# Performance work log

Hardware: AMD Instinct MI355X
Metric: run time of the kernel (lower is better)

## Reference

```python
import jax, jax.numpy as jnp
import numpy as np

HEADS = 16
NUM_CHUNKS = 8  # min(int(log2(4096))+1, 8)


def setup_inputs() -> dict:
    key = jax.random.key(0)
    ks = jax.random.split(key, 6)
    B, T, C = 4, 4096, 1024
    s = 1.0 / np.sqrt(C)
    x = jax.random.normal(ks[0], (B, T, C), jnp.float32)
    Wqkv = jax.random.normal(ks[1], (3 * C, C), jnp.float32) * s
    Wout = jax.random.normal(ks[2], (C, C), jnp.float32) * s
    bout = jnp.zeros((C,), jnp.float32)
    Wl1 = jax.random.normal(ks[3], (64, 1), jnp.float32)
    bl1 = jnp.zeros((64,), jnp.float32)
    Wl2 = jax.random.normal(ks[4], (HEADS, 64), jnp.float32) * 0.125
    bl2 = jnp.zeros((HEADS,), jnp.float32)
    return dict(x=x, Wqkv=Wqkv, Wout=Wout, bout=bout, Wl1=Wl1, bl1=bl1, Wl2=Wl2, bl2=bl2)


def reference(x, Wqkv, Wout, bout, Wl1, bl1, Wl2, bl2):
    B, T, C = x.shape
    H = HEADS
    dh = C // H
    nc = NUM_CHUNKS
    cs = T // nc
    scale = dh ** (-0.5)

    # qkv projection (torch Linear: x @ W.T), split, to [B,H,T,dh]
    qkv = x @ Wqkv.T  # [B,T,3C]
    q, k, v = jnp.split(qkv, 3, axis=-1)
    def heads(t):
        return t.reshape(B, T, H, dh).transpose(0, 2, 1, 3)
    q, k, v = heads(q), heads(k), heads(v)

    # lambda gates from log positions: [T,1] -> [T,H] -> [H,T]
    log_pos = jnp.log(jnp.arange(T, dtype=jnp.float32) + 1.0)[:, None]
    h1 = jax.nn.relu(log_pos @ Wl1.T + bl1)            # [T,64]
    lam = jax.nn.sigmoid(h1 @ Wl2.T + bl2).T           # [H,T]
    lam = lam.reshape(H, nc, cs)                        # per-chunk key gates

    # block-local (chunked) attention, fully vectorized over chunks
    qc = q.reshape(B, H, nc, cs, dh)
    kc = k.reshape(B, H, nc, cs, dh)
    vc = v.reshape(B, H, nc, cs, dh)
    scores = jnp.einsum('bhnqd,bhnkd->bhnqk', qc, kc) * scale
    scores = scores * lam[None, :, :, None, :]          # gate keys pre-softmax
    attn = jax.nn.softmax(scores, axis=-1)
    out = jnp.einsum('bhnqk,bhnkd->bhnqd', attn, vc)    # [B,H,nc,cs,dh]

    out = out.reshape(B, H, T, dh).transpose(0, 2, 1, 3).reshape(B, T, C)
    return out @ Wout.T + bout
```

## Files before the change

### kernel.cpp

```cpp
#include <hip/hip_runtime.h>
#include <hip/hip_bf16.h>

typedef unsigned short u16;
typedef __attribute__((ext_vector_type(8))) short v8s;
typedef __attribute__((ext_vector_type(4))) float v4f;
typedef __attribute__((ext_vector_type(16))) float v16f;
typedef __attribute__((ext_vector_type(4))) unsigned v4u;

#define DEV __device__ __forceinline__

DEV u16 f2bf(float f) {
  union { float f; unsigned u; } v; v.f = f;
  unsigned r = v.u + 0x7fffu + ((v.u >> 16) & 1u);
  return (u16)(r >> 16);
}

DEV unsigned pk2bf(float a, float b) {
  float2 t; t.x = a; t.y = b;
  __hip_bfloat162 p = __float22bfloat162_rn(t);
  union { __hip_bfloat162 h; unsigned u; } c; c.h = p;
  return c.u;
}

DEV void gload_lds16(const void* g, void* l) {
  __builtin_amdgcn_global_load_lds(
      (const __attribute__((address_space(1))) void*)g,
      (__attribute__((address_space(3))) void*)l, 16, 0, 0);
}

__global__ __launch_bounds__(256) void cvt_bf16(const float* __restrict__ in,
                                                u16* __restrict__ out, int n4) {
  int i = blockIdx.x * 256 + threadIdx.x;
  if (i >= n4) return;
  float4 v = ((const float4*)in)[i];
  ushort4 o;
  o.x = f2bf(v.x); o.y = f2bf(v.y); o.z = f2bf(v.z); o.w = f2bf(v.w);
  ((ushort4*)out)[i] = o;
}

__global__ __launch_bounds__(256) void lam_kernel(const float* __restrict__ Wl1,
    const float* __restrict__ bl1, const float* __restrict__ Wl2,
    const float* __restrict__ bl2, float* __restrict__ lam) {
  int t = blockIdx.x * 256 + threadIdx.x;
  float lp = logf((float)t + 1.0f);
  float h1[64];
#pragma unroll
  for (int j = 0; j < 64; ++j) h1[j] = fmaxf(lp * Wl1[j] + bl1[j], 0.0f);
#pragma unroll 1
  for (int h = 0; h < 16; ++h) {
    float z = bl2[h];
#pragma unroll
    for (int j = 0; j < 64; ++j) z += h1[j] * Wl2[h * 64 + j];
    lam[h * 4096 + t] = 0.125f / (1.0f + expf(-z));
  }
}

template <int MH>
DEV void mfma32(v4f (&acc)[8][4], const v8s (&a)[4][2], const v8s (&b)[4][2]) {
#pragma unroll
  for (int kk = 0; kk < 2; ++kk)
#pragma unroll
    for (int i = 0; i < 4; ++i)
#pragma unroll
      for (int j = 0; j < 4; ++j)
        acc[MH * 4 + i][j] = __builtin_amdgcn_mfma_f32_16x16x32_bf16(
            a[i][kk], b[j][kk], acc[MH * 4 + i][j], 0, 0, 0);
}

DEV void ldA(v8s (&a)[4][2], const u16* Ab, int wr, int mh, int lane) {
  const int l15 = lane & 15, g = lane >> 4;
#pragma unroll
  for (int i = 0; i < 4; ++i) {
    const int row = wr * 128 + mh * 64 + i * 16 + l15;
#pragma unroll
    for (int kk = 0; kk < 2; ++kk)
      a[i][kk] = *(const v8s*)(Ab + row * 64 + (((kk * 4 + g) ^ (row & 7)) << 3));
  }
}

DEV void ldB4(v8s (&b)[4][2], const u16* Bb, int wc, int lane) {
  const int l15 = lane & 15, g = lane >> 4;
#pragma unroll
  for (int j = 0; j < 4; ++j) {
    const int row = (j >> 1) * 128 + wc * 32 + (j & 1) * 16 + l15;
#pragma unroll
    for (int kk = 0; kk < 2; ++kk)
      b[j][kk] = *(const v8s*)(Bb + row * 64 + (((kk * 4 + g) ^ (row & 7)) << 3));
  }
}

template <int OUTF32>
__global__ __launch_bounds__(512, 2) void gemm256(const u16* __restrict__ A,
    const u16* __restrict__ Bt, void* __restrict__ Cout,
    const float* __restrict__ bias, int M, int N, int K) {
  __shared__ u16 As[2][256 * 64];
  __shared__ u16 Bs[2][256 * 64];
  const int tid = threadIdx.x;
  const int lane = tid & 63;
  const int nbn = N >> 8;
  const int nwg = gridDim.x;
  int wg = blockIdx.x;
  wg = (wg & 7) * (nwg >> 3) + (wg >> 3);
  const int m0 = (wg / nbn) << 8;
  const int n0 = (wg % nbn) << 8;
  const int wid = tid >> 6;
  const int wr = wid >> 2;
  const int wc = wid & 3;
  const int nkt = K >> 6;
  const int nit = nkt >> 1;

  auto SAu = [&](int buf, int kt, int u) {
    const int ur = tid >> 3;
    const int slot = (tid & 7) ^ (ur & 7);
    gload_lds16(A + (size_t)(m0 + u * 64 + ur) * K + kt * 64 + slot * 8,
                &As[buf][u * 4096 + (tid & ~63) * 8]);
  };
  auto SBu = [&](int buf, int kt, int u) {
    const int q = tid >> 3;
    const int grow = (((u & 1) * 2 + (q >> 5)) << 6) + ((u >> 1) << 5) + (q & 31);
    const int slot = (tid & 7) ^ (q & 7);
    gload_lds16(Bt + (size_t)(n0 + grow) * K + kt * 64 + slot * 8,
                &Bs[buf][u * 4096 + (tid & ~63) * 8]);
  };
  auto SA_ = [&](int buf, int kt, int mh) { SAu(buf, kt, mh); SAu(buf, kt, 2 + mh); };
  auto SB_ = [&](int buf, int kt, int nh) { SBu(buf, kt, nh * 2); SBu(buf, kt, nh * 2 + 1); };

  v4f acc[8][4] = {};
  v8s a0[4][2], a1[4][2], b[4][2];

  SA_(0, 0, 0); SA_(0, 0, 1); SB_(0, 0, 0); SB_(0, 0, 1);
  SA_(1, 1, 0); SB_(1, 1, 0); SB_(1, 1, 1);
  asm volatile("s_waitcnt vmcnt(6)" ::: "memory");
  asm volatile("s_barrier" ::: "memory");

#define PHASE(MHc, AREG, VM, ...)                           \
  do { __VA_ARGS__; } while (0);                            \
  __builtin_amdgcn_s_setprio(1);                            \
  mfma32<MHc>(acc, AREG, b);                                \
  __builtin_amdgcn_s_setprio(0);                            \
  if (VM) asm volatile("s_waitcnt vmcnt(6)" ::: "memory");  \
  asm volatile("s_barrier" ::: "memory");

  for (int it = 0; it < nit; ++it) {
    const int t0 = 2 * it;
    const int t1 = t0 + 1;
    const int t2 = (t0 + 2 < nkt) ? t0 + 2 : nkt - 1;
    const int t3 = (t0 + 3 < nkt) ? t0 + 3 : nkt - 1;
    ldA(a0, As[0], wr, 0, lane); ldB4(b, Bs[0], wc, lane);
    ldA(a1, As[0], wr, 1, lane);
    PHASE(0, a0, 0, SAu(1, t1, 1); SAu(1, t1, 3));
    PHASE(1, a1, 1, SB_(0, t2, 0); SB_(0, t2, 1); SAu(0, t2, 0); SAu(0, t2, 2));
    ldA(a0, As[1], wr, 0, lane); ldB4(b, Bs[1], wc, lane);
    ldA(a1, As[1], wr, 1, lane);
    PHASE(0, a0, 0, SAu(0, t2, 1); SAu(0, t2, 3));
    PHASE(1, a1, 1, SB_(1, t3, 0); SB_(1, t3, 1); SAu(1, t3, 0); SAu(1, t3, 2));
  }
#undef PHASE

  const int l15 = lane & 15, g4 = (lane >> 4) * 4;
#pragma unroll
  for (int i = 0; i < 8; ++i) {
#pragma unroll
    for (int j = 0; j < 4; ++j) {
      const int gr = m0 + wr * 128 + i * 16 + g4;
      const int gc = n0 + wc * 64 + j * 16 + l15;
      float bv = OUTF32 ? bias[gc] : 0.0f;
#pragma unroll
      for (int r = 0; r < 4; ++r) {
        float val = acc[i][j][r];
        if (OUTF32) ((float*)Cout)[(size_t)(gr + r) * N + gc] = val + bv;
        else ((u16*)Cout)[(size_t)(gr + r) * N + gc] = f2bf(val);
      }
    }
  }
}

__global__ __launch_bounds__(1024, 4) void attn_chunk(const u16* __restrict__ qkv,
    const float* __restrict__ lam, u16* __restrict__ aout) {
  __shared__ u16 Ksm[512 * 64];
  __shared__ u16 Vt[64 * 520];
  __shared__ float lam_s[512];

  const int tid = threadIdx.x;
  const int lane = tid & 63;
  const int wid = tid >> 6;
  const int blk = blockIdx.x;
  const int c = blk & 7;
  const int hd = (blk >> 3) & 15;
  const int b = blk >> 7;
  const size_t tok0 = (size_t)b * 4096 + c * 512;
  const u16* qb = qkv + tok0 * 3072 + hd * 64;
  const u16* kb = qb + 1024;
  const u16* vb = qb + 2048;

  if (tid < 512) lam_s[tid] = lam[hd * 4096 + c * 512 + tid];

#pragma unroll
  for (int i = 0; i < 4; ++i) {
    const int r = i * 128 + wid * 8 + (lane >> 3);
    const int f = (r & 3) | (((r >> 3) & 1) << 2);
    gload_lds16(kb + (size_t)r * 3072 + (((lane & 7) ^ f) << 3),
                &Ksm[(i * 128 + wid * 8) * 64]);
  }
  {
    const int pr = tid & 255;
    const int k0 = 2 * pr;
    const int kg = k0 & 31;
    const int col = (k0 & ~31) + (kg & 16) + (((kg >> 2) & 1) << 3) +
                    ((kg & 3) | ((kg & 8) >> 1));
    const int db0 = (tid >> 8) * 2;
#pragma unroll
    for (int dbi = 0; dbi < 2; ++dbi) {
      const int d0 = (db0 + dbi) * 8;
      v8s v0 = *(const v8s*)(vb + (size_t)k0 * 3072 + d0);
      v8s v1 = *(const v8s*)(vb + (size_t)(k0 + 1) * 3072 + d0);
#pragma unroll
      for (int j = 0; j < 8; ++j) {
        unsigned pk = (unsigned)(u16)v0[j] | ((unsigned)(u16)v1[j] << 16);
        *(unsigned*)&Vt[(d0 + j) * 520 + col] = pk;
      }
    }
  }
  __syncthreads();

  const int l31 = lane & 31;
  const int hf = lane >> 5;
  const int fk = (l31 & 3) | (((l31 >> 3) & 1) << 2);

  const int q0 = wid * 32;
  v8s qv[4];
#pragma unroll
  for (int dsec = 0; dsec < 4; ++dsec)
    qv[dsec] = *(const v8s*)(qb + (size_t)(q0 + l31) * 3072 + dsec * 16 + hf * 8);

  float m = -1e30f, sum = 0.0f;
  v16f o0 = {}, o1 = {};

#pragma unroll 1
  for (int kt = 0; kt < 16; ++kt) {
    v16f acc = {};
#pragma unroll
    for (int dsec = 0; dsec < 4; ++dsec) {
      const v8s kf = *(const v8s*)&Ksm[(kt * 32 + l31) * 64 +
                                       (((dsec * 2 + hf) ^ fk) << 3)];
      acc = __builtin_amdgcn_mfma_f32_32x32x16_bf16(kf, qv[dsec], acc, 0, 0, 0);
    }
#pragma unroll
    for (int a = 0; a < 4; ++a) {
      const v4f lv = *(const v4f*)&lam_s[kt * 32 + a * 8 + hf * 4];
#pragma unroll
      for (int i = 0; i < 4; ++i) acc[4 * a + i] *= lv[i];
    }
    float tm = acc[0];
#pragma unroll
    for (int r = 1; r < 16; ++r) tm = fmaxf(tm, acc[r]);
    tm = fmaxf(tm, __shfl_xor(tm, 32));
    if (!__all(tm <= m + 8.0f)) {
      const float nm = fmaxf(m, tm);
      const float sc = __expf(m - nm);
      sum *= sc;
      o0 *= sc; o1 *= sc;
      m = nm;
    }
    float ps = 0.0f;
#pragma unroll
    for (int r = 0; r < 16; ++r) { acc[r] = __expf(acc[r] - m); ps += acc[r]; }
    sum += ps;
    v4u pa, pb;
    pa.x = pk2bf(acc[0], acc[1]);   pa.y = pk2bf(acc[2], acc[3]);
    pa.z = pk2bf(acc[4], acc[5]);   pa.w = pk2bf(acc[6], acc[7]);
    pb.x = pk2bf(acc[8], acc[9]);   pb.y = pk2bf(acc[10], acc[11]);
    pb.z = pk2bf(acc[12], acc[13]); pb.w = pk2bf(acc[14], acc[15]);
    const v8s pfA = __builtin_bit_cast(v8s, pa);
    const v8s pfB = __builtin_bit_cast(v8s, pb);
    const int vcol = kt * 32 + hf * 8;
    const v8s vA0 = *(const v8s*)&Vt[l31 * 520 + vcol];
    const v8s vB0 = *(const v8s*)&Vt[l31 * 520 + vcol + 16];
    const v8s vA1 = *(const v8s*)&Vt[(32 + l31) * 520 + vcol];
    const v8s vB1 = *(const v8s*)&Vt[(32 + l31) * 520 + vcol + 16];
    o0 = __builtin_amdgcn_mfma_f32_32x32x16_bf16(vA0, pfA, o0, 0, 0, 0);
    o0 = __builtin_amdgcn_mfma_f32_32x32x16_bf16(vB0, pfB, o0, 0, 0, 0);
    o1 = __builtin_amdgcn_mfma_f32_32x32x16_bf16(vA1, pfA, o1, 0, 0, 0);
    o1 = __builtin_amdgcn_mfma_f32_32x32x16_bf16(vB1, pfB, o1, 0, 0, 0);
  }

  sum += __shfl_xor(sum, 32);
  const float sv = 1.0f / sum;

  const size_t obase = (tok0 + q0 + l31) * 1024 + hd * 64;
#pragma unroll
  for (int a = 0; a < 4; ++a) {
    ushort4 w0, w1;
    w0.x = f2bf(o0[4 * a + 0] * sv); w0.y = f2bf(o0[4 * a + 1] * sv);
    w0.z = f2bf(o0[4 * a + 2] * sv); w0.w = f2bf(o0[4 * a + 3] * sv);
    w1.x = f2bf(o1[4 * a + 0] * sv); w1.y = f2bf(o1[4 * a + 1] * sv);
    w1.z = f2bf(o1[4 * a + 2] * sv); w1.w = f2bf(o1[4 * a + 3] * sv);
    *(ushort4*)&aout[obase + 8 * a + 4 * hf] = w0;
    *(ushort4*)&aout[obase + 32 + 8 * a + 4 * hf] = w1;
  }
}

extern "C" void kernel_launch(void* const* d_in, const int* in_sizes, int n_in,
                              void* d_out, int out_size, void* d_ws, size_t ws_size,
                              hipStream_t stream) {
  const float* x    = (const float*)d_in[0];
  const float* Wqkv = (const float*)d_in[1];
  const float* Wout = (const float*)d_in[2];
  const float* bout = (const float*)d_in[3];
  const float* Wl1  = (const float*)d_in[4];
  const float* bl1  = (const float*)d_in[5];
  const float* Wl2  = (const float*)d_in[6];
  const float* bl2  = (const float*)d_in[7];
  float* out = (float*)d_out;

  char* ws = (char*)d_ws;
  u16* xbf    = (u16*)ws; ws += (size_t)16384 * 1024 * 2;
  u16* wqkvbf = (u16*)ws; ws += (size_t)3072 * 1024 * 2;
  u16* woutbf = (u16*)ws; ws += (size_t)1024 * 1024 * 2;
  u16* qkvbf  = (u16*)ws; ws += (size_t)16384 * 3072 * 2;
  u16* aoutbf = (u16*)ws; ws += (size_t)16384 * 1024 * 2;
  float* lam  = (float*)ws; ws += (size_t)16 * 4096 * 4;

  cvt_bf16<<<16384, 256, 0, stream>>>(x, xbf, 16777216 / 4);
  cvt_bf16<<<3072, 256, 0, stream>>>(Wqkv, wqkvbf, 3145728 / 4);
  cvt_bf16<<<1024, 256, 0, stream>>>(Wout, woutbf, 1048576 / 4);
  lam_kernel<<<16, 256, 0, stream>>>(Wl1, bl1, Wl2, bl2, lam);

  gemm256<0><<<dim3((16384 / 256) * (3072 / 256)), 512, 0, stream>>>(
      xbf, wqkvbf, qkvbf, nullptr, 16384, 3072, 1024);

  attn_chunk<<<512, 1024, 0, stream>>>(qkvbf, lam, aoutbf);

  gemm256<1><<<dim3((16384 / 256) * (1024 / 256)), 512, 0, stream>>>(
      aoutbf, woutbf, out, bout, 16384, 1024, 1024);
}
```

Before: 244.7 us.

## Replace 256x256 GEMM with 128x256 tile, BK=32 triple-buffered pipeline

Both projection GEMMs move from a 256x256 tile with a 64-wide K step and double buffering to a 128x256 tile with a 32-wide K step and a three-stage LDS ring. The smaller footprint allows four workgroups per CU and doubles the grid, aiming at better occupancy and latency hiding. The cost is lower arithmetic intensity per tile, more global traffic for B, and a barrier on every 32-wide K step.

Result: slower. 266.3 us (+8.8%).

```diff
diff --git a/kernel.cpp b/kernel.cpp
--- a/kernel.cpp
+++ b/kernel.cpp
@@ -55,114 +55,82 @@
   }
 }
 
-template <int MH>
-DEV void mfma32(v4f (&acc)[8][4], const v8s (&a)[4][2], const v8s (&b)[4][2]) {
-#pragma unroll
-  for (int kk = 0; kk < 2; ++kk)
-#pragma unroll
-    for (int i = 0; i < 4; ++i)
-#pragma unroll
-      for (int j = 0; j < 4; ++j)
-        acc[MH * 4 + i][j] = __builtin_amdgcn_mfma_f32_16x16x32_bf16(
-            a[i][kk], b[j][kk], acc[MH * 4 + i][j], 0, 0, 0);
-}
-
-DEV void ldA(v8s (&a)[4][2], const u16* Ab, int wr, int mh, int lane) {
-  const int l15 = lane & 15, g = lane >> 4;
-#pragma unroll
-  for (int i = 0; i < 4; ++i) {
-    const int row = wr * 128 + mh * 64 + i * 16 + l15;
-#pragma unroll
-    for (int kk = 0; kk < 2; ++kk)
-      a[i][kk] = *(const v8s*)(Ab + row * 64 + (((kk * 4 + g) ^ (row & 7)) << 3));
-  }
-}
-
-DEV void ldB4(v8s (&b)[4][2], const u16* Bb, int wc, int lane) {
-  const int l15 = lane & 15, g = lane >> 4;
-#pragma unroll
-  for (int j = 0; j < 4; ++j) {
-    const int row = (j >> 1) * 128 + wc * 32 + (j & 1) * 16 + l15;
-#pragma unroll
-    for (int kk = 0; kk < 2; ++kk)
-      b[j][kk] = *(const v8s*)(Bb + row * 64 + (((kk * 4 + g) ^ (row & 7)) << 3));
-  }
-}
-
 template <int OUTF32>
-__global__ __launch_bounds__(512, 2) void gemm256(const u16* __restrict__ A,
+__global__ __launch_bounds__(512, 4) void gemm128(const u16* __restrict__ A,
     const u16* __restrict__ Bt, void* __restrict__ Cout,
     const float* __restrict__ bias, int M, int N, int K) {
-  __shared__ u16 As[2][256 * 64];
-  __shared__ u16 Bs[2][256 * 64];
+  __shared__ u16 As[3][128 * 32];
+  __shared__ u16 Bs[3][256 * 32];
   const int tid = threadIdx.x;
   const int lane = tid & 63;
   const int nbn = N >> 8;
   const int nwg = gridDim.x;
   int wg = blockIdx.x;
   wg = (wg & 7) * (nwg >> 3) + (wg >> 3);
-  const int m0 = (wg / nbn) << 8;
+  const int m0 = (wg / nbn) << 7;
   const int n0 = (wg % nbn) << 8;
   const int wid = tid >> 6;
   const int wr = wid >> 2;
   const int wc = wid & 3;
-  const int nkt = K >> 6;
-  const int nit = nkt >> 1;
-
-  auto SAu = [&](int buf, int kt, int u) {
-    const int ur = tid >> 3;
-    const int slot = (tid & 7) ^ (ur & 7);
-    gload_lds16(A + (size_t)(m0 + u * 64 + ur) * K + kt * 64 + slot * 8,
-                &As[buf][u * 4096 + (tid & ~63) * 8]);
+  const int nkt = K >> 5;
+
+  const int srow = tid >> 2;
+  const int scol = ((tid & 3) ^ ((srow >> 1) & 3)) << 3;
+  auto SA = [&](int buf, int kt) {
+    gload_lds16(A + (size_t)(m0 + srow) * K + kt * 32 + scol,
+                &As[buf][(tid & ~63) * 8]);
   };
-  auto SBu = [&](int buf, int kt, int u) {
-    const int q = tid >> 3;
-    const int grow = (((u & 1) * 2 + (q >> 5)) << 6) + ((u >> 1) << 5) + (q & 31);
-    const int slot = (tid & 7) ^ (q & 7);
-    gload_lds16(Bt + (size_t)(n0 + grow) * K + kt * 64 + slot * 8,
+  auto SB = [&](int buf, int kt, int u) {
+    gload_lds16(Bt + (size_t)(n0 + u * 128 + srow) * K + kt * 32 + scol,
                 &Bs[buf][u * 4096 + (tid & ~63) * 8]);
   };
-  auto SA_ = [&](int buf, int kt, int mh) { SAu(buf, kt, mh); SAu(buf, kt, 2 + mh); };
-  auto SB_ = [&](int buf, int kt, int nh) { SBu(buf, kt, nh * 2); SBu(buf, kt, nh * 2 + 1); };
-
-  v4f acc[8][4] = {};
-  v8s a0[4][2], a1[4][2], b[4][2];
-
-  SA_(0, 0, 0); SA_(0, 0, 1); SB_(0, 0, 0); SB_(0, 0, 1);
-  SA_(1, 1, 0); SB_(1, 1, 0); SB_(1, 1, 1);
-  asm volatile("s_waitcnt vmcnt(6)" ::: "memory");
+  auto STAGE = [&](int buf, int kt) { SA(buf, kt); SB(buf, kt, 0); SB(buf, kt, 1); };
+
+  v4f acc[4][4] = {};
+  v8s a[4], b[4];
+
+  STAGE(0, 0);
+  STAGE(1, 1 < nkt ? 1 : 0);
+  asm volatile("s_waitcnt vmcnt(3)" ::: "memory");
   asm volatile("s_barrier" ::: "memory");
 
-#define PHASE(MHc, AREG, VM, ...)                           \
-  do { __VA_ARGS__; } while (0);                            \
-  __builtin_amdgcn_s_setprio(1);                            \
-  mfma32<MHc>(acc, AREG, b);                                \
-  __builtin_amdgcn_s_setprio(0);                            \
-  if (VM) asm volatile("s_waitcnt vmcnt(6)" ::: "memory");  \
-  asm volatile("s_barrier" ::: "memory");
-
-  for (int it = 0; it < nit; ++it) {
-    const int t0 = 2 * it;
-    const int t1 = t0 + 1;
-    const int t2 = (t0 + 2 < nkt) ? t0 + 2 : nkt - 1;
-    const int t3 = (t0 + 3 < nkt) ? t0 + 3 : nkt - 1;
-    ldA(a0, As[0], wr, 0, lane); ldB4(b, Bs[0], wc, lane);
-    ldA(a1, As[0], wr, 1, lane);
-    PHASE(0, a0, 0, SAu(1, t1, 1); SAu(1, t1, 3));
-    PHASE(1, a1, 1, SB_(0, t2, 0); SB_(0, t2, 1); SAu(0, t2, 0); SAu(0, t2, 2));
-    ldA(a0, As[1], wr, 0, lane); ldB4(b, Bs[1], wc, lane);
-    ldA(a1, As[1], wr, 1, lane);
-    PHASE(0, a0, 0, SAu(0, t2, 1); SAu(0, t2, 3));
-    PHASE(1, a1, 1, SB_(1, t3, 0); SB_(1, t3, 1); SAu(1, t3, 0); SAu(1, t3, 2));
-  }
-#undef PHASE
-
-  const int l15 = lane & 15, g4 = (lane >> 4) * 4;
-#pragma unroll
-  for (int i = 0; i < 8; ++i) {
+  const int l15 = lane & 15, g = lane >> 4;
+  const int fsl = (l15 >> 1) & 3;
+  const int aoff = ((g ^ fsl) << 3);
+
+#pragma unroll 1
+  for (int t = 0; t < nkt; ++t) {
+    const u16* Ab = As[t % 3];
+    const u16* Bb = Bs[t % 3];
+#pragma unroll
+    for (int i = 0; i < 4; ++i)
+      a[i] = *(const v8s*)(Ab + (wr * 64 + i * 16 + l15) * 32 + aoff);
+#pragma unroll
+    for (int j = 0; j < 4; ++j)
+      b[j] = *(const v8s*)(Bb + (wc * 64 + j * 16 + l15) * 32 + aoff);
+
+    const bool more = (t + 2 < nkt);
+    if (more) STAGE((t + 2) % 3, t + 2);
+
+    __builtin_amdgcn_s_setprio(1);
+#pragma unroll
+    for (int i = 0; i < 4; ++i)
+#pragma unroll
+      for (int j = 0; j < 4; ++j)
+        acc[i][j] = __builtin_amdgcn_mfma_f32_16x16x32_bf16(a[i], b[j],
+                                                            acc[i][j], 0, 0, 0);
+    __builtin_amdgcn_s_setprio(0);
+    if (more) asm volatile("s_waitcnt vmcnt(3)" ::: "memory");
+    else      asm volatile("s_waitcnt vmcnt(0)" ::: "memory");
+    asm volatile("s_barrier" ::: "memory");
+  }
+
+  const int g4 = g * 4;
+#pragma unroll
+  for (int i = 0; i < 4; ++i) {
 #pragma unroll
     for (int j = 0; j < 4; ++j) {
-      const int gr = m0 + wr * 128 + i * 16 + g4;
+      const int gr = m0 + wr * 64 + i * 16 + g4;
       const int gc = n0 + wc * 64 + j * 16 + l15;
       float bv = OUTF32 ? bias[gc] : 0.0f;
 #pragma unroll
@@ -326,11 +294,11 @@
   cvt_bf16<<<1024, 256, 0, stream>>>(Wout, woutbf, 1048576 / 4);
   lam_kernel<<<16, 256, 0, stream>>>(Wl1, bl1, Wl2, bl2, lam);
 
-  gemm256<0><<<dim3((16384 / 256) * (3072 / 256)), 512, 0, stream>>>(
+  gemm128<0><<<dim3(1536), 512, 0, stream>>>(
       xbf, wqkvbf, qkvbf, nullptr, 16384, 3072, 1024);
 
   attn_chunk<<<512, 1024, 0, stream>>>(qkvbf, lam, aoutbf);
 
-  gemm256<1><<<dim3((16384 / 256) * (1024 / 256)), 512, 0, stream>>>(
+  gemm128<1><<<dim3(512), 512, 0, stream>>>(
       aoutbf, woutbf, out, bout, 16384, 1024, 1024);
 }
```
